# Kernel optimization log

Hardware: AMD Instinct MI355X
Metric: run time of the kernel (lower is better)

## Reference

```python
import jax, jax.numpy as jnp
import numpy as np

OUT_FEATURES = 4096
IN_FEATURES = 4096
SCALE_EPS = 1e-5


def setup_inputs() -> dict:
    key = jax.random.key(0)
    k1, k2, k3 = jax.random.split(key, 3)
    x = jax.random.normal(k1, (8192, IN_FEATURES), dtype=jnp.float32)
    # packed int4 weights: two signed nibbles per byte-equivalent int
    weight_packed = jax.random.randint(k2, (OUT_FEATURES, IN_FEATURES // 2), 0, 256, dtype=jnp.int32)
    weight_scale = jax.random.uniform(k3, (OUT_FEATURES,), dtype=jnp.float32) * 0.01 + 1e-4
    return {"x": x, "weight_packed": weight_packed, "weight_scale": weight_scale}


def _unpack_int4(weight_packed):
    # low nibble first, then high nibble, sign-extended from 4 bits
    low = weight_packed & 15
    high = (weight_packed >> 4) & 15
    low = jnp.where(low > 7, low - 16, low)
    high = jnp.where(high > 7, high - 16, high)
    # interleave -> [out_features, in_features]
    w_q = jnp.stack([low, high], axis=-1).reshape(weight_packed.shape[0], -1)
    return w_q


def reference(x, weight_packed, weight_scale):
    # per-row activation quantization to int4 range [-8, 7]
    x_max = jnp.max(jnp.abs(x), axis=-1, keepdims=True)
    x_scale = jnp.maximum(x_max / 7.0, SCALE_EPS)          # [tokens, 1]
    x_q = jnp.clip(jnp.round(x / x_scale), -8.0, 7.0)      # float carrier of int4 values

    w_q = _unpack_int4(weight_packed).astype(jnp.float32)  # [out, in]

    out = jnp.einsum('ti,oi->to', x_q, w_q)                # [tokens, out]
    out = out * (x_scale * weight_scale[None, :])
    return out.astype(x.dtype)
```

## Files before the change

kernel.cpp:

```cpp
#include <hip/hip_runtime.h>

#define SCALE_EPS 1e-5f

typedef int v4i __attribute__((ext_vector_type(4)));

static __device__ __forceinline__ void gll16(const void* g, void* l) {
  __builtin_amdgcn_global_load_lds(
      (const __attribute__((address_space(1))) unsigned int*)g,
      (__attribute__((address_space(3))) unsigned int*)l,
      16, 0, 0);
}


__global__ __launch_bounds__(256) void unpack_w(const int* __restrict__ wp,
                                                char* __restrict__ wq) {
  const int kc = blockIdx.x;
  const int nt = blockIdx.y;
  const int tid = threadIdx.x;
  char* tile = wq + ((size_t)nt * 64 + kc) * 4096;
  const int n0 = nt * 128;
#pragma unroll
  for (int gi = 0; gi < 2; ++gi) {
    int g = gi * 256 + tid;
    int r = g >> 2, cc = g & 3;
    const v4i* src = (const v4i*)(wp + (size_t)(n0 + r) * 2048 + kc * 32 + cc * 8);
    v4i m0 = src[0], m1 = src[1];
    unsigned int d0 =
        ((unsigned)m0.x & 15) | (((unsigned)m0.z & 15) << 4) |
        ((((unsigned)m0.x >> 4) & 15) << 8) | ((((unsigned)m0.z >> 4) & 15) << 12) |
        (((unsigned)m0.y & 15) << 16) | (((unsigned)m0.w & 15) << 20) |
        ((((unsigned)m0.y >> 4) & 15) << 24) | ((((unsigned)m0.w >> 4) & 15) << 28);
    unsigned int d1 =
        ((unsigned)m1.x & 15) | (((unsigned)m1.z & 15) << 4) |
        ((((unsigned)m1.x >> 4) & 15) << 8) | ((((unsigned)m1.z >> 4) & 15) << 12) |
        (((unsigned)m1.y & 15) << 16) | (((unsigned)m1.w & 15) << 20) |
        ((((unsigned)m1.y >> 4) & 15) << 24) | ((((unsigned)m1.w >> 4) & 15) << 28);
    d0 ^= 0x88888888u;
    d1 ^= 0x88888888u;
    *(uint2*)(tile + (r >> 5) * 1024 + cc * 256 + (r & 15) * 16 + ((r >> 4) & 1) * 8) =
        make_uint2(d0, d1);
  }
}

__global__ __launch_bounds__(256) void sum_w(const int* __restrict__ wp,
                                             int* __restrict__ sw) {
  __shared__ int ls[4];
  const int row = blockIdx.x;
  const int tid = threadIdx.x;
  const v4i* src = (const v4i*)(wp + (size_t)row * 2048 + tid * 8);
  v4i m0 = src[0], m1 = src[1];
  int s = 0;
#pragma unroll
  for (int j = 0; j < 4; ++j) {
    int a = (j == 0) ? m0.x : (j == 1) ? m0.y : (j == 2) ? m0.z : m0.w;
    int b = (j == 0) ? m1.x : (j == 1) ? m1.y : (j == 2) ? m1.z : m1.w;
    s += ((a & 15) ^ 8) + (((a >> 4) & 15) ^ 8) + ((b & 15) ^ 8) + (((b >> 4) & 15) ^ 8);
  }
#pragma unroll
  for (int d = 1; d < 64; d <<= 1) s += __shfl_xor(s, d, 64);
  if ((tid & 63) == 0) ls[tid >> 6] = s;
  __syncthreads();
  if (tid == 0) sw[row] = ls[0] + ls[1] + ls[2] + ls[3];
}

__global__ __launch_bounds__(256) void quant_x(const float* __restrict__ x,
                                               char* __restrict__ xq,
                                               float* __restrict__ xs,
                                               int* __restrict__ sa) {
  __shared__ float lmax[4][4];
  __shared__ int lsum[4][4];
  const int tid = threadIdx.x;
  const int w = tid >> 6;
  const int l = tid & 63;
  const int t0 = blockIdx.x * 4;
  const int row = l >> 4;
  const int t = t0 + row;
  const int sub = l & 15;

  const float* base = x + (size_t)t * 4096 + w * 1024 + sub * 8;
  float4 va[8], vb[8];
  float m = 0.0f;
#pragma unroll
  for (int s = 0; s < 8; ++s) {
    va[s] = *(const float4*)(base + s * 128);
    vb[s] = *(const float4*)(base + s * 128 + 4);
    m = fmaxf(m, fmaxf(fmaxf(fabsf(va[s].x), fabsf(va[s].y)),
                       fmaxf(fabsf(va[s].z), fabsf(va[s].w))));
    m = fmaxf(m, fmaxf(fmaxf(fabsf(vb[s].x), fabsf(vb[s].y)),
                       fmaxf(fabsf(vb[s].z), fabsf(vb[s].w))));
  }
#pragma unroll
  for (int d = 1; d < 16; d <<= 1) m = fmaxf(m, __shfl_xor(m, d, 64));
  if (sub == 0) lmax[w][row] = m;
  __syncthreads();
  float rm = fmaxf(fmaxf(lmax[0][row], lmax[1][row]),
                   fmaxf(lmax[2][row], lmax[3][row]));
  float scale = fmaxf(rm / 7.0f, SCALE_EPS);
  if (w == 0 && sub == 0) xs[t] = scale;

  const int mt = t >> 7;
  const int f = (t & 127) >> 4;
  const int r16 = t & 15;
  const int cc = (sub >> 1) & 3;
  const int d = sub & 1;
  char* dst0 = xq + (size_t)(mt * 64) * 4096 +
               (f >> 1) * 1024 + cc * 256 + r16 * 16 + (f & 1) * 8 + d * 4;

  int isum = 0;
#pragma unroll
  for (int s = 0; s < 8; ++s) {
    int q0 = (int)fminf(fmaxf(rintf(va[s].x / scale), -8.0f), 7.0f) + 8;
    int q1 = (int)fminf(fmaxf(rintf(va[s].y / scale), -8.0f), 7.0f) + 8;
    int q2 = (int)fminf(fmaxf(rintf(va[s].z / scale), -8.0f), 7.0f) + 8;
    int q3 = (int)fminf(fmaxf(rintf(va[s].w / scale), -8.0f), 7.0f) + 8;
    int q4 = (int)fminf(fmaxf(rintf(vb[s].x / scale), -8.0f), 7.0f) + 8;
    int q5 = (int)fminf(fmaxf(rintf(vb[s].y / scale), -8.0f), 7.0f) + 8;
    int q6 = (int)fminf(fmaxf(rintf(vb[s].z / scale), -8.0f), 7.0f) + 8;
    int q7 = (int)fminf(fmaxf(rintf(vb[s].w / scale), -8.0f), 7.0f) + 8;
    isum += q0 + q1 + q2 + q3 + q4 + q5 + q6 + q7;
    unsigned int dw = (unsigned)(q0 | (q4 << 4)) | ((unsigned)(q1 | (q5 << 4)) << 8) |
                      ((unsigned)(q2 | (q6 << 4)) << 16) | ((unsigned)(q3 | (q7 << 4)) << 24);
    int kc = w * 16 + s * 2 + (sub >> 3);
    *(unsigned int*)(dst0 + (size_t)kc * 4096) = dw;
  }
#pragma unroll
  for (int dd = 1; dd < 16; dd <<= 1) isum += __shfl_xor(isum, dd, 64);
  if (sub == 0) lsum[w][row] = isum;
  __syncthreads();
  if (w == 0 && sub == 0)
    sa[t] = lsum[0][row] + lsum[1][row] + lsum[2][row] + lsum[3][row];
}

__global__ __launch_bounds__(512, 2) void gemm_i8(const char* __restrict__ xq,
                                                  const char* __restrict__ wq,
                                                  const float* __restrict__ xs,
                                                  const int* __restrict__ sa,
                                                  const int* __restrict__ sw,
                                                  const float* __restrict__ wsc,
                                                  float* __restrict__ out) {
  __shared__ char lds[4][16384];
  const int tid = threadIdx.x;
  const int wid = tid >> 6;
  const int lane = tid & 63;
  const int wm = wid >> 2;
  const int wn = wid & 3;

  const int bid = blockIdx.x;
  const int wg = (bid & 7) * 64 + (bid >> 3);
  const int by = wg >> 4;
  const int bx = wg & 15;

  const int toff = tid * 16;
  const int h = toff >> 12;
  const int off = toff & 4095;
  const char* aSrcT = xq + (size_t)(2 * by + h) * 262144 + off;
  const char* bSrcT = wq + (size_t)(2 * bx + h) * 262144 + off;
  const int aoff = (lane >> 4) * 256 + (lane & 15) * 16;

  v4i acc[8][4] = {};
  v4i fB[2][4];
  v4i pA0, pA1, pB0, pB1;
  v4i ua0, ua1, ua2, ua3;

#define LO4(w) (int)((unsigned)(w) & 0x0f0f0f0fu)
#define HI4(w) (int)(((unsigned)(w) >> 4) & 0x0f0f0f0fu)
#define UNPK(da, db, p)                                   \
  do {                                                    \
    da = (v4i){LO4((p).x), HI4((p).x), LO4((p).y), HI4((p).y)}; \
    db = (v4i){LO4((p).z), HI4((p).z), LO4((p).w), HI4((p).w)}; \
  } while (0)

#define STAGE2(kt)                                        \
  do {                                                    \
    char* d_ = lds[(kt) & 3] + toff;                      \
    gll16(aSrcT + (size_t)(kt) * 4096, d_);               \
    gll16(bSrcT + (size_t)(kt) * 4096, d_ + 8192);        \
  } while (0)

#define MF2(m0, m1, xx, yy, c)                                                         \
  do {                                                                                 \
    __builtin_amdgcn_s_setprio(1);                                                     \
    _Pragma("unroll") for (int ni = 0; ni < 4; ++ni) {                                 \
      acc[m0][ni] =                                                                    \
          __builtin_amdgcn_mfma_i32_16x16x64_i8(xx, fB[c][ni], acc[m0][ni], 0, 0, 0);  \
      acc[m1][ni] =                                                                    \
          __builtin_amdgcn_mfma_i32_16x16x64_i8(yy, fB[c][ni], acc[m1][ni], 0, 0, 0);  \
    }                                                                                  \
    __builtin_amdgcn_s_setprio(0);                                                     \
  } while (0)

#define TILE(c, kt, do_stage, do_next, vm)                                   \
  do {                                                                       \
    const char* Aw_ = lds[(kt) & 3] + wm * 4096 + aoff;                      \
    const char* Bn_ = lds[((kt) + 1) & 3] + 8192 + wn * 2048 + aoff;         \
    const char* An_ = lds[((kt) + 1) & 3] + wm * 4096 + aoff;                \
                                \
    pA1 = *(const v4i*)(Aw_ + 1024);                                         \
    UNPK(ua0, ua1, pA0);                                                     \
    MF2(0, 1, ua0, ua1, c);                                                  \
                                \
    pA0 = *(const v4i*)(Aw_ + 2048);                                         \
    UNPK(ua2, ua3, pA1);                                                     \
    MF2(2, 3, ua2, ua3, c);                                                  \
                           \
    if ((vm) == 2) asm volatile("s_waitcnt vmcnt(2)" ::: "memory");          \
    else if ((vm) == 0) asm volatile("s_waitcnt vmcnt(0)" ::: "memory");     \
    __builtin_amdgcn_s_barrier();                                            \
    __builtin_amdgcn_sched_barrier(0);                                       \
          \
    if (do_stage) STAGE2((kt) + 3);                                          \
    pA1 = *(const v4i*)(Aw_ + 3072);                                         \
    if (do_next) pB0 = *(const v4i*)(Bn_);                                   \
    UNPK(ua0, ua1, pA0);                                                     \
    MF2(4, 5, ua0, ua1, c);                                                  \
       \
    if (do_next) {                                                           \
      pB1 = *(const v4i*)(Bn_ + 1024);                                       \
      pA0 = *(const v4i*)(An_);                                              \
    }                                                                        \
    UNPK(ua2, ua3, pA1);                                                     \
    MF2(6, 7, ua2, ua3, c);                                                  \
    if (do_next) {                                                           \
      UNPK(fB[1 - (c)][0], fB[1 - (c)][1], pB0);                             \
      UNPK(fB[1 - (c)][2], fB[1 - (c)][3], pB1);                             \
    }                                                                        \
  } while (0)

  STAGE2(0); STAGE2(1); STAGE2(2);
  asm volatile("s_waitcnt vmcnt(4)" ::: "memory");
  __builtin_amdgcn_s_barrier();
  __builtin_amdgcn_sched_barrier(0);
  {
    const char* B0_ = lds[0] + 8192 + wn * 2048 + aoff;
    pB0 = *(const v4i*)(B0_);
    pB1 = *(const v4i*)(B0_ + 1024);
    pA0 = *(const v4i*)(lds[0] + wm * 4096 + aoff);
    UNPK(fB[0][0], fB[0][1], pB0);
    UNPK(fB[0][2], fB[0][3], pB1);
  }

  for (int kt = 0; kt < 60; kt += 2) {
    TILE(0, kt, 1, 1, 2);
    TILE(1, kt + 1, 1, 1, 2);
  }
  TILE(0, 60, 1, 1, 2);
  TILE(1, 61, 0, 1, 2);
  TILE(0, 62, 0, 1, 0);
  TILE(1, 63, 0, 0, -1);

#undef TILE
#undef MF2
#undef STAGE2
#undef UNPK
#undef LO4
#undef HI4

  int swv[4];
  float wvv[4];
#pragma unroll
  for (int ni = 0; ni < 4; ++ni) {
    int col = bx * 256 + wn * 64 + ni * 16 + (lane & 15);
    swv[ni] = sw[col];
    wvv[ni] = wsc[col];
  }
  const int rbase = by * 256 + wm * 128 + ((lane >> 4) << 2);
  const int cbase = bx * 256 + wn * 64 + (lane & 15);
#pragma unroll
  for (int mi = 0; mi < 8; ++mi) {
#pragma unroll
    for (int j = 0; j < 4; ++j) {
      int t = rbase + mi * 16 + j;
      int sat = sa[t];
      float xsv = xs[t];
      float* orow = out + (size_t)t * 4096 + cbase;
#pragma unroll
      for (int ni = 0; ni < 4; ++ni) {
        int cv = acc[mi][ni][j] - 8 * (sat + swv[ni]) + 262144;
        orow[ni * 16] = (float)cv * (xsv * wvv[ni]);
      }
    }
  }
}

extern "C" void kernel_launch(void* const* d_in, const int* in_sizes, int n_in,
                              void* d_out, int out_size, void* d_ws, size_t ws_size,
                              hipStream_t stream) {
  const float* x = (const float*)d_in[0];
  const int* wp = (const int*)d_in[1];
  const float* wsc = (const float*)d_in[2];
  float* out = (float*)d_out;
  char* ws = (char*)d_ws;

  char* xq = ws;
  char* wq = ws + 16777216;
  float* xs = (float*)(ws + 25165824);
  int* sa = (int*)(ws + 25165824 + 32768);
  int* sw = (int*)(ws + 25165824 + 65536);

  hipLaunchKernelGGL(unpack_w, dim3(64, 32), dim3(256), 0, stream, wp, wq);
  hipLaunchKernelGGL(sum_w, dim3(4096), dim3(256), 0, stream, wp, sw);
  hipLaunchKernelGGL(quant_x, dim3(2048), dim3(256), 0, stream, x, xq, xs, sa);
  hipLaunchKernelGGL(gemm_i8, dim3(512), dim3(512), 0, stream, xq, wq, xs, sa, sw, wsc, out);
}
```

Before: 165.0 us.

## Switch int8 GEMM to 32x32x32 MFMA with matching packed operand layout

Replaces the 16x16x64 i8 MFMA tiles with 32x32x32 i8 MFMA, so each wave holds a 4x2 grid of 32x32 accumulators. The packed int4 layouts written by unpack_w and quant_x are reorganized into 256-row, 8KB-per-k-chunk tiles to match the new fragment shape. The goal is fewer MFMA issues and fewer LDS fragment reads per k-step, with higher operand reuse per instruction. The epilogue and the pre-pass indexing are rewritten to fit, and the quant_x row sum now counts signed values instead of offset ones, which changes the zero-point correction arithmetic.

Result: no change. 164.1 us (-0.6%).

```diff
diff --git a/kernel.cpp b/kernel.cpp
--- a/kernel.cpp
+++ b/kernel.cpp
@@ -3,6 +3,7 @@
 #define SCALE_EPS 1e-5f
 
 typedef int v4i __attribute__((ext_vector_type(4)));
+typedef int v16i __attribute__((ext_vector_type(16)));
 
 static __device__ __forceinline__ void gll16(const void* g, void* l) {
   __builtin_amdgcn_global_load_lds(
@@ -15,30 +16,23 @@
 __global__ __launch_bounds__(256) void unpack_w(const int* __restrict__ wp,
                                                 char* __restrict__ wq) {
   const int kc = blockIdx.x;
-  const int nt = blockIdx.y;
-  const int tid = threadIdx.x;
-  char* tile = wq + ((size_t)nt * 64 + kc) * 4096;
-  const int n0 = nt * 128;
-#pragma unroll
-  for (int gi = 0; gi < 2; ++gi) {
-    int g = gi * 256 + tid;
-    int r = g >> 2, cc = g & 3;
-    const v4i* src = (const v4i*)(wp + (size_t)(n0 + r) * 2048 + kc * 32 + cc * 8);
-    v4i m0 = src[0], m1 = src[1];
-    unsigned int d0 =
-        ((unsigned)m0.x & 15) | (((unsigned)m0.z & 15) << 4) |
-        ((((unsigned)m0.x >> 4) & 15) << 8) | ((((unsigned)m0.z >> 4) & 15) << 12) |
-        (((unsigned)m0.y & 15) << 16) | (((unsigned)m0.w & 15) << 20) |
-        ((((unsigned)m0.y >> 4) & 15) << 24) | ((((unsigned)m0.w >> 4) & 15) << 28);
-    unsigned int d1 =
-        ((unsigned)m1.x & 15) | (((unsigned)m1.z & 15) << 4) |
-        ((((unsigned)m1.x >> 4) & 15) << 8) | ((((unsigned)m1.z >> 4) & 15) << 12) |
-        (((unsigned)m1.y & 15) << 16) | (((unsigned)m1.w & 15) << 20) |
-        ((((unsigned)m1.y >> 4) & 15) << 24) | ((((unsigned)m1.w >> 4) & 15) << 28);
-    d0 ^= 0x88888888u;
-    d1 ^= 0x88888888u;
-    *(uint2*)(tile + (r >> 5) * 1024 + cc * 256 + (r & 15) * 16 + ((r >> 4) & 1) * 8) =
-        make_uint2(d0, d1);
+  const int nt2 = blockIdx.y;
+  const int tid = threadIdx.x;
+  char* tile = wq + ((size_t)nt2 * 64 + kc) * 8192;
+#pragma unroll
+  for (int it = 0; it < 8; ++it) {
+    int idx = it * 256 + tid;
+    int c = idx >> 3;
+    int rem = idx & 7;
+    int kh = rem >> 2, q = rem & 3;
+    const int* src = wp + (size_t)(nt2 * 256 + c) * 2048 + kc * 32 + kh * 8 + q * 2;
+    int i0 = src[0], i1 = src[1], j0 = src[16], j1 = src[17];
+    unsigned dw = ((unsigned)i0 & 15) | (((unsigned)j0 & 15) << 4) |
+                  ((((unsigned)i0 >> 4) & 15) << 8) | ((((unsigned)j0 >> 4) & 15) << 12) |
+                  (((unsigned)i1 & 15) << 16) | (((unsigned)j1 & 15) << 20) |
+                  ((((unsigned)i1 >> 4) & 15) << 24) | ((((unsigned)j1 >> 4) & 15) << 28);
+    dw ^= 0x88888888u;
+    *(unsigned*)(tile + (c >> 5) * 1024 + (kh * 32 + (c & 31)) * 16 + q * 4) = dw;
   }
 }
 
@@ -76,14 +70,18 @@
   const int row = l >> 4;
   const int t = t0 + row;
   const int sub = l & 15;
-
-  const float* base = x + (size_t)t * 4096 + w * 1024 + sub * 8;
+  const int kcl = sub >> 3;
+  const int kh = (sub >> 2) & 1;
+  const int j = sub & 3;
+
   float4 va[8], vb[8];
   float m = 0.0f;
 #pragma unroll
   for (int s = 0; s < 8; ++s) {
-    va[s] = *(const float4*)(base + s * 128);
-    vb[s] = *(const float4*)(base + s * 128 + 4);
+    int kc = w * 16 + s * 2 + kcl;
+    const float* p = x + (size_t)t * 4096 + kc * 64 + kh * 16 + j * 4;
+    va[s] = *(const float4*)(p);
+    vb[s] = *(const float4*)(p + 32);
     m = fmaxf(m, fmaxf(fmaxf(fabsf(va[s].x), fabsf(va[s].y)),
                        fmaxf(fabsf(va[s].z), fabsf(va[s].w))));
     m = fmaxf(m, fmaxf(fmaxf(fabsf(vb[s].x), fabsf(vb[s].y)),
@@ -98,30 +96,27 @@
   float scale = fmaxf(rm / 7.0f, SCALE_EPS);
   if (w == 0 && sub == 0) xs[t] = scale;
 
-  const int mt = t >> 7;
-  const int f = (t & 127) >> 4;
-  const int r16 = t & 15;
-  const int cc = (sub >> 1) & 3;
-  const int d = sub & 1;
-  char* dst0 = xq + (size_t)(mt * 64) * 4096 +
-               (f >> 1) * 1024 + cc * 256 + r16 * 16 + (f & 1) * 8 + d * 4;
+  char* dst0 = xq + (size_t)(t >> 8) * 524288 + ((t & 255) >> 5) * 1024 +
+               (kh * 32 + (t & 31)) * 16 + j * 4;
 
   int isum = 0;
 #pragma unroll
   for (int s = 0; s < 8; ++s) {
-    int q0 = (int)fminf(fmaxf(rintf(va[s].x / scale), -8.0f), 7.0f) + 8;
-    int q1 = (int)fminf(fmaxf(rintf(va[s].y / scale), -8.0f), 7.0f) + 8;
-    int q2 = (int)fminf(fmaxf(rintf(va[s].z / scale), -8.0f), 7.0f) + 8;
-    int q3 = (int)fminf(fmaxf(rintf(va[s].w / scale), -8.0f), 7.0f) + 8;
-    int q4 = (int)fminf(fmaxf(rintf(vb[s].x / scale), -8.0f), 7.0f) + 8;
-    int q5 = (int)fminf(fmaxf(rintf(vb[s].y / scale), -8.0f), 7.0f) + 8;
-    int q6 = (int)fminf(fmaxf(rintf(vb[s].z / scale), -8.0f), 7.0f) + 8;
-    int q7 = (int)fminf(fmaxf(rintf(vb[s].w / scale), -8.0f), 7.0f) + 8;
+    int kc = w * 16 + s * 2 + kcl;
+    int q0 = (int)fminf(fmaxf(rintf(va[s].x / scale), -8.0f), 7.0f);
+    int q1 = (int)fminf(fmaxf(rintf(va[s].y / scale), -8.0f), 7.0f);
+    int q2 = (int)fminf(fmaxf(rintf(va[s].z / scale), -8.0f), 7.0f);
+    int q3 = (int)fminf(fmaxf(rintf(va[s].w / scale), -8.0f), 7.0f);
+    int q4 = (int)fminf(fmaxf(rintf(vb[s].x / scale), -8.0f), 7.0f);
+    int q5 = (int)fminf(fmaxf(rintf(vb[s].y / scale), -8.0f), 7.0f);
+    int q6 = (int)fminf(fmaxf(rintf(vb[s].z / scale), -8.0f), 7.0f);
+    int q7 = (int)fminf(fmaxf(rintf(vb[s].w / scale), -8.0f), 7.0f);
     isum += q0 + q1 + q2 + q3 + q4 + q5 + q6 + q7;
-    unsigned int dw = (unsigned)(q0 | (q4 << 4)) | ((unsigned)(q1 | (q5 << 4)) << 8) |
-                      ((unsigned)(q2 | (q6 << 4)) << 16) | ((unsigned)(q3 | (q7 << 4)) << 24);
-    int kc = w * 16 + s * 2 + (sub >> 3);
-    *(unsigned int*)(dst0 + (size_t)kc * 4096) = dw;
+    unsigned dw = (unsigned)((q0 + 8) | ((q4 + 8) << 4)) |
+                  ((unsigned)((q1 + 8) | ((q5 + 8) << 4)) << 8) |
+                  ((unsigned)((q2 + 8) | ((q6 + 8) << 4)) << 16) |
+                  ((unsigned)((q3 + 8) | ((q7 + 8) << 4)) << 24);
+    *(unsigned*)(dst0 + (size_t)kc * 8192) = dw;
   }
 #pragma unroll
   for (int dd = 1; dd < 16; dd <<= 1) isum += __shfl_xor(isum, dd, 64);
@@ -151,78 +146,74 @@
   const int bx = wg & 15;
 
   const int toff = tid * 16;
-  const int h = toff >> 12;
-  const int off = toff & 4095;
-  const char* aSrcT = xq + (size_t)(2 * by + h) * 262144 + off;
-  const char* bSrcT = wq + (size_t)(2 * bx + h) * 262144 + off;
-  const int aoff = (lane >> 4) * 256 + (lane & 15) * 16;
-
-  v4i acc[8][4] = {};
-  v4i fB[2][4];
-  v4i pA0, pA1, pB0, pB1;
-  v4i ua0, ua1, ua2, ua3;
-
-#define LO4(w) (int)((unsigned)(w) & 0x0f0f0f0fu)
-#define HI4(w) (int)(((unsigned)(w) >> 4) & 0x0f0f0f0fu)
-#define UNPK(da, db, p)                                   \
-  do {                                                    \
-    da = (v4i){LO4((p).x), HI4((p).x), LO4((p).y), HI4((p).y)}; \
-    db = (v4i){LO4((p).z), HI4((p).z), LO4((p).w), HI4((p).w)}; \
-  } while (0)
-
-#define STAGE2(kt)                                        \
-  do {                                                    \
-    char* d_ = lds[(kt) & 3] + toff;                      \
-    gll16(aSrcT + (size_t)(kt) * 4096, d_);               \
-    gll16(bSrcT + (size_t)(kt) * 4096, d_ + 8192);        \
-  } while (0)
-
-#define MF2(m0, m1, xx, yy, c)                                                         \
-  do {                                                                                 \
-    __builtin_amdgcn_s_setprio(1);                                                     \
-    _Pragma("unroll") for (int ni = 0; ni < 4; ++ni) {                                 \
-      acc[m0][ni] =                                                                    \
-          __builtin_amdgcn_mfma_i32_16x16x64_i8(xx, fB[c][ni], acc[m0][ni], 0, 0, 0);  \
-      acc[m1][ni] =                                                                    \
-          __builtin_amdgcn_mfma_i32_16x16x64_i8(yy, fB[c][ni], acc[m1][ni], 0, 0, 0);  \
-    }                                                                                  \
-    __builtin_amdgcn_s_setprio(0);                                                     \
-  } while (0)
-
-#define TILE(c, kt, do_stage, do_next, vm)                                   \
+  const char* aSrc = xq + (size_t)by * 524288;
+  const char* bSrc = wq + (size_t)bx * 524288;
+  const int laoff = lane * 16;
+
+  v16i acc[4][2] = {};
+  v4i pA0, pA1, pA2, pA3, pB0, pB1;
+  v4i a00, a01, a10, a11, a20, a21, a30, a31;
+  v4i b00, b01, b10, b11;
+  const unsigned MSK = 0x0f0f0f0fu;
+
+#define LO4(w) (int)((unsigned)(w) & MSK)
+#define HI4(w) (int)(((unsigned)(w) >> 4) & MSK)
+#define UNPK(d0, d1, p)                                        \
+  do {                                                         \
+    d0 = (v4i){LO4((p).x), LO4((p).y), LO4((p).z), LO4((p).w)}; \
+    d1 = (v4i){HI4((p).x), HI4((p).y), HI4((p).z), HI4((p).w)}; \
+  } while (0)
+
+#define STAGE2(kt)                                             \
+  do {                                                         \
+    char* d_ = lds[(kt) & 3] + toff;                           \
+    gll16(aSrc + (size_t)(kt) * 8192 + toff, d_);              \
+    gll16(bSrc + (size_t)(kt) * 8192 + toff, d_ + 8192);       \
+  } while (0)
+
+#define CL(rb, xx, yy, bA, bB)                                                 \
+  do {                                                                         \
+    __builtin_amdgcn_s_setprio(1);                                             \
+    acc[rb][0] = __builtin_amdgcn_mfma_i32_32x32x32_i8(xx, bA, acc[rb][0], 0, 0, 0);   \
+    acc[rb][1] = __builtin_amdgcn_mfma_i32_32x32x32_i8(xx, bB, acc[rb][1], 0, 0, 0);   \
+    acc[rb + 1][0] = __builtin_amdgcn_mfma_i32_32x32x32_i8(yy, bA, acc[rb + 1][0], 0, 0, 0); \
+    acc[rb + 1][1] = __builtin_amdgcn_mfma_i32_32x32x32_i8(yy, bB, acc[rb + 1][1], 0, 0, 0); \
+    __builtin_amdgcn_s_setprio(0);                                             \
+  } while (0)
+
+#define TILE(kt, do_stage, do_next, vm)                                      \
   do {                                                                       \
-    const char* Aw_ = lds[(kt) & 3] + wm * 4096 + aoff;                      \
-    const char* Bn_ = lds[((kt) + 1) & 3] + 8192 + wn * 2048 + aoff;         \
-    const char* An_ = lds[((kt) + 1) & 3] + wm * 4096 + aoff;                \
-                                \
-    pA1 = *(const v4i*)(Aw_ + 1024);                                         \
-    UNPK(ua0, ua1, pA0);                                                     \
-    MF2(0, 1, ua0, ua1, c);                                                  \
-                                \
-    pA0 = *(const v4i*)(Aw_ + 2048);                                         \
-    UNPK(ua2, ua3, pA1);                                                     \
-    MF2(2, 3, ua2, ua3, c);                                                  \
-                           \
+    const char* An_ = lds[((kt) + 1) & 3] + wm * 4096 + laoff;               \
+    const char* Bn_ = lds[((kt) + 1) & 3] + 8192 + wn * 2048 + laoff;        \
+     \
+    UNPK(a20, a21, pA2);                                                     \
+    UNPK(a30, a31, pA3);                                                     \
+    CL(0, a00, a10, b00, b10);                                               \
+    CL(2, a20, a30, b00, b10);                                               \
+                            \
     if ((vm) == 2) asm volatile("s_waitcnt vmcnt(2)" ::: "memory");          \
     else if ((vm) == 0) asm volatile("s_waitcnt vmcnt(0)" ::: "memory");     \
     __builtin_amdgcn_s_barrier();                                            \
     __builtin_amdgcn_sched_barrier(0);                                       \
-          \
+      \
     if (do_stage) STAGE2((kt) + 3);                                          \
-    pA1 = *(const v4i*)(Aw_ + 3072);                                         \
-    if (do_next) pB0 = *(const v4i*)(Bn_);                                   \
-    UNPK(ua0, ua1, pA0);                                                     \
-    MF2(4, 5, ua0, ua1, c);                                                  \
-       \
     if (do_next) {                                                           \
+      pA0 = *(const v4i*)(An_);                                              \
+      pA1 = *(const v4i*)(An_ + 1024);                                       \
+      pB0 = *(const v4i*)(Bn_);                                              \
       pB1 = *(const v4i*)(Bn_ + 1024);                                       \
-      pA0 = *(const v4i*)(An_);                                              \
     }                                                                        \
-    UNPK(ua2, ua3, pA1);                                                     \
-    MF2(6, 7, ua2, ua3, c);                                                  \
+    CL(0, a01, a11, b01, b11);                                               \
     if (do_next) {                                                           \
-      UNPK(fB[1 - (c)][0], fB[1 - (c)][1], pB0);                             \
-      UNPK(fB[1 - (c)][2], fB[1 - (c)][3], pB1);                             \
+      pA2 = *(const v4i*)(An_ + 2048);                                       \
+      pA3 = *(const v4i*)(An_ + 3072);                                       \
+    }                                                                        \
+    CL(2, a21, a31, b01, b11);                                               \
+    if (do_next) {                                                           \
+      UNPK(a00, a01, pA0);                                                   \
+      UNPK(a10, a11, pA1);                                                   \
+      UNPK(b00, b01, pB0);                                                   \
+      UNPK(b10, b11, pB1);                                                   \
     }                                                                        \
   } while (0)
 
@@ -231,52 +222,55 @@
   __builtin_amdgcn_s_barrier();
   __builtin_amdgcn_sched_barrier(0);
   {
-    const char* B0_ = lds[0] + 8192 + wn * 2048 + aoff;
+    const char* A0_ = lds[0] + wm * 4096 + laoff;
+    const char* B0_ = lds[0] + 8192 + wn * 2048 + laoff;
+    pA0 = *(const v4i*)(A0_);
+    pA1 = *(const v4i*)(A0_ + 1024);
+    pA2 = *(const v4i*)(A0_ + 2048);
+    pA3 = *(const v4i*)(A0_ + 3072);
     pB0 = *(const v4i*)(B0_);
     pB1 = *(const v4i*)(B0_ + 1024);
-    pA0 = *(const v4i*)(lds[0] + wm * 4096 + aoff);
-    UNPK(fB[0][0], fB[0][1], pB0);
-    UNPK(fB[0][2], fB[0][3], pB1);
+    UNPK(a00, a01, pA0);
+    UNPK(a10, a11, pA1);
+    UNPK(b00, b01, pB0);
+    UNPK(b10, b11, pB1);
   }
 
   for (int kt = 0; kt < 60; kt += 2) {
-    TILE(0, kt, 1, 1, 2);
-    TILE(1, kt + 1, 1, 1, 2);
-  }
-  TILE(0, 60, 1, 1, 2);
-  TILE(1, 61, 0, 1, 2);
-  TILE(0, 62, 0, 1, 0);
-  TILE(1, 63, 0, 0, -1);
+    TILE(kt, 1, 1, 2);
+    TILE(kt + 1, 1, 1, 2);
+  }
+  TILE(60, 1, 1, 2);
+  TILE(61, 0, 1, 2);
+  TILE(62, 0, 1, 0);
+  TILE(63, 0, 0, -1);
 
 #undef TILE
-#undef MF2
+#undef CL
 #undef STAGE2
 #undef UNPK
 #undef LO4
 #undef HI4
 
-  int swv[4];
-  float wvv[4];
-#pragma unroll
-  for (int ni = 0; ni < 4; ++ni) {
-    int col = bx * 256 + wn * 64 + ni * 16 + (lane & 15);
-    swv[ni] = sw[col];
-    wvv[ni] = wsc[col];
-  }
-  const int rbase = by * 256 + wm * 128 + ((lane >> 4) << 2);
-  const int cbase = bx * 256 + wn * 64 + (lane & 15);
-#pragma unroll
-  for (int mi = 0; mi < 8; ++mi) {
-#pragma unroll
-    for (int j = 0; j < 4; ++j) {
-      int t = rbase + mi * 16 + j;
-      int sat = sa[t];
-      float xsv = xs[t];
-      float* orow = out + (size_t)t * 4096 + cbase;
-#pragma unroll
-      for (int ni = 0; ni < 4; ++ni) {
-        int cv = acc[mi][ni][j] - 8 * (sat + swv[ni]) + 262144;
-        orow[ni * 16] = (float)cv * (xsv * wvv[ni]);
+  const int colb = bx * 256 + wn * 64 + (lane & 31);
+  int sw0 = sw[colb];
+  int sw1 = sw[colb + 32];
+  float wv0 = wsc[colb];
+  float wv1 = wsc[colb + 32];
+  const int rw = by * 256 + wm * 128 + ((lane >> 5) << 2);
+#pragma unroll
+  for (int rb = 0; rb < 4; ++rb) {
+#pragma unroll
+    for (int g = 0; g < 4; ++g) {
+#pragma unroll
+      for (int j = 0; j < 4; ++j) {
+        int r = rw + rb * 32 + g * 8 + j;
+        int reg = g * 4 + j;
+        int sv = sa[r];
+        float s = xs[r];
+        float* orow = out + (size_t)r * 4096 + colb;
+        orow[0]  = (float)(acc[rb][0][reg] - 8 * (sv + sw0)) * (s * wv0);
+        orow[32] = (float)(acc[rb][1][reg] - 8 * (sv + sw1)) * (s * wv1);
       }
     }
   }
@@ -297,7 +291,7 @@
   int* sa = (int*)(ws + 25165824 + 32768);
   int* sw = (int*)(ws + 25165824 + 65536);
 
-  hipLaunchKernelGGL(unpack_w, dim3(64, 32), dim3(256), 0, stream, wp, wq);
+  hipLaunchKernelGGL(unpack_w, dim3(64, 16), dim3(256), 0, stream, wp, wq);
   hipLaunchKernelGGL(sum_w, dim3(4096), dim3(256), 0, stream, wp, sw);
   hipLaunchKernelGGL(quant_x, dim3(2048), dim3(256), 0, stream, x, xq, xs, sa);
   hipLaunchKernelGGL(gemm_i8, dim3(512), dim3(512), 0, stream, xq, wq, xs, sa, sw, wsc, out);
```
